# Performance work log

Hardware: AMD Instinct MI355X
Metric: run time of the kernel (lower is better)

Reference implementation:

```python
import jax, jax.numpy as jnp
import numpy as np

STEPS = 100
VTH = 1.0
POOL_TH = 0.75


def _conv(x, w):
    # 5x5 conv, stride 1, pad 2, no bias; NCHW / OIHW
    return jax.lax.conv_general_dilated(
        x, w, window_strides=(1, 1), padding=[(2, 2), (2, 2)],
        dimension_numbers=('NCHW', 'OIHW', 'NCHW'))


def _avgpool2(x):
    s = jax.lax.reduce_window(x, 0.0, jax.lax.add, (1, 1, 2, 2), (1, 1, 2, 2), 'VALID')
    return s * 0.25


def _fire(mem, th):
    # torch.nn.functional.threshold(mem, th, 0): keep values > th, else 0
    ex = jnp.where(mem > th, mem, 0.0)
    mem = mem - ex
    out = (ex > 0).astype(mem.dtype)
    return mem, out


def _ave(output, inp):
    c = inp >= output
    denom = jnp.sum(jnp.where(c, inp, 0.0))
    num = jnp.sum(jnp.where(c, output, 0.0))
    return jnp.where(denom < 1e-3, 1.0, num / denom)


def _ave_p(output, inp):
    denom = jnp.sum(inp)
    return jnp.where(denom < 1e-3, 1.0, jnp.sum(output) / denom)


def setup_inputs() -> dict:
    key = jax.random.key(0)
    k_in, k1, k2, k3, k4 = jax.random.split(key, 5)
    B = 512
    inputdata = jax.random.uniform(k_in, (B, 1, 28, 28), dtype=jnp.float32)
    w1 = jax.random.normal(k1, (20, 1, 5, 5), dtype=jnp.float32) * np.sqrt(2.0 / (5 * 5 * 1))
    w2 = jax.random.normal(k2, (50, 20, 5, 5), dtype=jnp.float32) * np.sqrt(2.0 / (5 * 5 * 20))
    wf0 = jax.random.normal(k3, (200, 2450), dtype=jnp.float32) * np.sqrt(2.0 / 2450)
    wf1 = jax.random.normal(k4, (10, 200), dtype=jnp.float32) * np.sqrt(2.0 / 200)
    return {'inputdata': inputdata, 'w1': w1, 'w2': w2, 'wf0': wf0, 'wf1': wf1}


def _spiking_loop(inputdata, w1, w2, wf0, wf1):
    B = inputdata.shape[0]
    f32 = jnp.float32
    z = lambda *s: jnp.zeros(s, f32)
    carry0 = (
        z(B, 20, 28, 28), z(B, 20, 14, 14), z(B, 50, 14, 14), z(B, 50, 7, 7), z(B, 200),  # membranes
        z(B, 1, 28, 28),                                                                   # Total_input
        z(B, 20, 28, 28), z(B, 20, 28, 28),   # Total_1_output, IF_in_c1
        z(B, 20, 14, 14), z(B, 20, 14, 14),   # Total_p1_output, IF_in_p1
        z(B, 50, 14, 14), z(B, 50, 14, 14),   # Total_2_output, IF_in_c2
        z(B, 50, 7, 7), z(B, 50, 7, 7),       # Total_p2_output, IF_in_p2
        z(B, 200), z(B, 200),                  # Total_f0_output, IF_in_f0
    )

    sgn = jnp.sign(inputdata)
    half = jnp.abs(inputdata) / 2.0

    def step(carry, k):
        (m1, m1s, m2, m2s, mf0, Tin, T1, IFc1, Tp1, IFp1, T2, IFc2, Tp2, IFp2, Tf0, IFf0) = carry
        r = jax.random.uniform(k, inputdata.shape, dtype=f32)
        poisson = (half > r).astype(f32) * sgn
        Tin = Tin + poisson

        a = _conv(poisson, w1)
        m1 = m1 + a
        m1, o = _fire(m1, VTH)            # LIF (l=1 -> membrane unchanged)
        IFc1 = IFc1 + a
        T1 = T1 + o

        a = _avgpool2(o)
        m1s = m1s + a
        m1s, o = _fire(m1s, POOL_TH)
        IFp1 = IFp1 + a
        Tp1 = Tp1 + o

        a = _conv(o, w2)
        m2 = m2 + a
        m2, o = _fire(m2, VTH)
        IFc2 = IFc2 + a
        T2 = T2 + o

        a = _avgpool2(o)
        m2s = m2s + a
        m2s, o = _fire(m2s, POOL_TH)
        IFp2 = IFp2 + a
        Tp2 = Tp2 + o

        a = o.reshape(B, -1) @ wf0.T
        mf0 = mf0 + a
        mf0, o = _fire(mf0, VTH)
        IFf0 = IFf0 + a
        Tf0 = Tf0 + o

        return (m1, m1s, m2, m2s, mf0, Tin, T1, IFc1, Tp1, IFp1, T2, IFc2, Tp2, IFp2, Tf0, IFf0), None

    keys = jax.random.split(jax.random.key(42), STEPS)
    carry, _ = jax.lax.scan(step, carry0, keys)
    return jax.lax.stop_gradient(carry)  # loop ran under torch.no_grad()


def _forward(inputdata, w1, w2, wf0, wf1):
    sg = jax.lax.stop_gradient
    (_, _, _, _, _, Tin, T1, IFc1, Tp1, IFp1, T2, IFc2, Tp2, IFp2, Tf0, IFf0) = \
        _spiking_loop(inputdata, w1, w2, wf0, wf1)

    # global scales start at 1, sign == 1 branch taken
    s1 = 0.6 * _ave(T1, IFc1) + 0.4
    s2 = 0.6 * _ave_p(Tp1, IFp1) + 0.4
    s3 = 0.6 * _ave(T2, IFc2) + 0.4
    s4 = 0.6 * _ave_p(Tp2, IFp2) + 0.4
    s5 = 0.6 * _ave(Tf0, IFf0) + 0.4
    sc1 = s1 * (IFc1 > 0).astype(jnp.float32)
    sc2 = s2 * (IFp1 > 0).astype(jnp.float32)
    sc3 = s3 * (IFc2 > 0).astype(jnp.float32)
    sc4 = s4 * (IFp2 > 0).astype(jnp.float32)
    sc5 = s5 * (IFf0 > 0).astype(jnp.float32)

    # straight-through graph (ASF-BP)
    B = inputdata.shape[0]
    o = _conv(Tin, w1) * sc1
    T1g = o - sg(o) + T1
    o = _avgpool2(T1g) * sc2
    Tp1g = o - sg(o) + Tp1
    o = _conv(Tp1g, w2) * sc3
    T2g = o - sg(o) + T2
    o = _avgpool2(T2g) * sc4
    Tp2g = o - sg(o) + Tp2
    o = (Tp2g.reshape(B, -1) @ wf0.T) * sc5
    Tf0g = o - sg(o) + Tf0
    fc1_in = Tf0g @ wf1.T
    return fc1_in / VTH / STEPS


def reference(inputdata, w1, w2, wf0, wf1):
    return _forward(inputdata, w1, w2, wf0, wf1)
```

## Files before the change

### kernel.cpp

```cpp
#include <hip/hip_runtime.h>
#include <stdint.h>

#define STEPS 100

typedef float f2 __attribute__((ext_vector_type(2)));

__device__ __forceinline__ uint32_t rotl32(uint32_t v, int r) {
  return (v << r) | (v >> (32 - r));
}

__device__ __forceinline__ void tf2x32(uint32_t k0, uint32_t k1,
                                       uint32_t x0, uint32_t x1,
                                       uint32_t& o0, uint32_t& o1) {
  uint32_t ks2 = k0 ^ k1 ^ 0x1BD11BDAu;
  x0 += k0; x1 += k1;
#define RND(r) { x0 += x1; x1 = rotl32(x1, (r)); x1 ^= x0; }
  RND(13) RND(15) RND(26) RND(6)
  x0 += k1;  x1 += ks2 + 1u;
  RND(17) RND(29) RND(16) RND(24)
  x0 += ks2; x1 += k0 + 2u;
  RND(13) RND(15) RND(26) RND(6)
  x0 += k0;  x1 += k1 + 3u;
  RND(17) RND(29) RND(16) RND(24)
  x0 += k1;  x1 += ks2 + 4u;
  RND(13) RND(15) RND(26) RND(6)
  x0 += ks2; x1 += k0 + 5u;
#undef RND
  o0 = x0; o1 = x1;
}

__global__ void keys_k(uint32_t* __restrict__ kb) {
  int i = threadIdx.x;
  if (i < STEPS) {
    uint32_t a, b;
    tf2x32(0u, 42u, 0u, (uint32_t)i, a, b);
    kb[2 * i] = a;
    kb[2 * i + 1] = b;
  }
}

__global__ void wt_k(const float* __restrict__ w2, float* __restrict__ wT2) {
  int i = blockIdx.x * blockDim.x + threadIdx.x;
  if (i >= 50 * 560) return;
  int oc = i / 560, r = i % 560;
  int ic = r / 28, j = r % 28;
  wT2[i] = (j < 25) ? w2[oc * 500 + ic * 25 + j] : 0.f;
}

__global__ void wf0t_k(const float* __restrict__ wf0,
                       float* __restrict__ wf0T) {
  int i = blockIdx.x * blockDim.x + threadIdx.x;
  if (i >= 2450 * 256) return;
  int k = i >> 8, n = i & 255;
  wf0T[i] = (n < 200) ? wf0[n * 2450 + k] : 0.f;
}

template <int KY>
__device__ __forceinline__ void p2s(const float4& q0, const float4& q1,
                                    const float4& q2, const float4& q3,
                                    const float (&wv)[28], f2 (&a)[7]) {
  f2 E[8] = {{q0.x, q0.y}, {q0.z, q0.w}, {q1.x, q1.y}, {q1.z, q1.w},
             {q2.x, q2.y}, {q2.z, q2.w}, {q3.x, q3.y}, {q3.z, q3.w}};
  f2 O[8] = {{q0.y, q0.z}, {q0.w, q1.x}, {q1.y, q1.z}, {q1.w, q2.x},
             {q2.y, q2.z}, {q2.w, q3.x}, {q3.y, q3.z}, {q3.w, 0.f}};
  constexpr int K = KY * 5;
  f2 W;
  W = f2{wv[K + 0], wv[K + 0]};
#pragma unroll
  for (int j = 0; j < 7; ++j) a[j] = __builtin_elementwise_fma(W, E[j], a[j]);
  W = f2{wv[K + 1], wv[K + 1]};
#pragma unroll
  for (int j = 0; j < 7; ++j) a[j] = __builtin_elementwise_fma(W, O[j], a[j]);
  W = f2{wv[K + 2], wv[K + 2]};
#pragma unroll
  for (int j = 0; j < 7; ++j) a[j] = __builtin_elementwise_fma(W, E[j + 1], a[j]);
  W = f2{wv[K + 3], wv[K + 3]};
#pragma unroll
  for (int j = 0; j < 7; ++j) a[j] = __builtin_elementwise_fma(W, O[j + 1], a[j]);
  W = f2{wv[K + 4], wv[K + 4]};
#pragma unroll
  for (int j = 0; j < 6; ++j) a[j] = __builtin_elementwise_fma(W, E[j + 2], a[j]);
}

__global__ __launch_bounds__(512, 2) void step_all_k(
    const float* __restrict__ x, const float* __restrict__ w1,
    const float* __restrict__ wT2, const uint32_t* __restrict__ kb,
    uint32_t* __restrict__ sp2g) {
  __shared__ __align__(16) float  xhs_l[784];
  __shared__ __align__(16) float  pois_l[32 * 34];
  __shared__ __align__(16) float  sp1_l[20 * 18 * 20];
  __shared__ int8_t  s2_l[50 * 196];
  __shared__ __align__(16) float  m2_l[50 * 196];
  __shared__ float    m2s_l[2450];
  __shared__ float    m1s_l[20 * 196];
  __shared__ float    m1stash[512 * 21];

  const int b  = blockIdx.x;
  const int t  = threadIdx.x;
  const int lq = t & 255;
  const int ohu = __builtin_amdgcn_readfirstlane(t >> 8);
  const bool act1 = lq < 196;
  const int qy = lq / 14, qx = lq % 14;
  const bool pair2 = t < 192;
  const bool sing2 = (t >= 192) && (t < 508);
  const int ocP = t / 7;
  const int y0P = 2 * (t % 7);
  const int gS  = 384 + (t - 192);
  const int ocS = gS / 14;
  const int yS  = gS % 14;

  for (int p = t; p < 784; p += 512) {
    xhs_l[p] = x[b * 784 + p] * 0.5f;
  }
  for (int i = t; i < 32 * 34; i += 512) pois_l[i] = 0.f;
  for (int i = t; i < 20 * 360; i += 512) sp1_l[i] = 0.f;
  for (int i = t; i < 50 * 196; i += 512) m2_l[i] = 0.f;
  for (int i = t; i < 2450; i += 512) m2s_l[i] = 0.f;
  for (int i = t; i < 20 * 196; i += 512) m1s_l[i] = 0.f;
  for (int i = t; i < 512 * 21; i += 512) m1stash[i] = 0.f;

  float m1p[2][10];
#pragma unroll
  for (int i = 0; i < 10; ++i) {
    m1p[0][i] = 0.f;
    m1p[1][i] = 0.f;
  }
  __syncthreads();

  {
    uint32_t k0 = kb[0], k1 = kb[1];
    for (int p = t; p < 784; p += 512) {
      uint32_t o0, o1;
      tf2x32(k0, k1, 0u, (uint32_t)(b * 784 + p), o0, o1);
      float r = __uint_as_float(((o0 ^ o1) >> 9) | 0x3F800000u) - 1.0f;
      float v = xhs_l[p];
      pois_l[(p / 28 + 2) * 34 + (p % 28 + 2)] =
          (fabsf(v) > r) ? ((v > 0.f) ? 1.f : -1.f) : 0.f;
    }
  }
  __syncthreads();

#define LDROW(rr, d) {                                                      \
    const float2* _pr = reinterpret_cast<const float2*>(                    \
        &pois_l[(2 * qy + (rr)) * 34 + 2 * qx]);                            \
    float2 _a0 = _pr[0], _a1 = _pr[1], _a2 = _pr[2];                        \
    d[0] = _a0.x; d[1] = _a0.y; d[2] = _a1.x;                               \
    d[3] = _a1.y; d[4] = _a2.x; d[5] = _a2.y; }

#define LD4(icv, rowv, p0, p1, p2, p3) {                                    \
    const float4* _rn = reinterpret_cast<const float4*>(                    \
        sp1_l + (icv) * 360 + (rowv) * 20);                                 \
    p0 = _rn[0]; p1 = _rn[1]; p2 = _rn[2]; p3 = _rn[3]; }

  for (int s = 0; s < STEPS; ++s) {
    if (act1) {
      float rA[6], rB[6];
      LDROW(0, rA)
      LDROW(1, rB)
      float acc[4][10];
#pragma unroll
      for (int tt = 0; tt < 4; ++tt)
#pragma unroll
        for (int i = 0; i < 10; ++i) acc[tt][i] = 0.f;
#pragma unroll
      for (int ky = 0; ky < 5; ++ky) {
#pragma unroll
        for (int kx = 0; kx < 5; ++kx) {
#pragma unroll
          for (int i = 0; i < 10; ++i) {
            float w = w1[(ohu * 10 + i) * 25 + ky * 5 + kx];
            acc[0][i] += w * rA[kx];
            acc[1][i] += w * rA[kx + 1];
            acc[2][i] += w * rB[kx];
            acc[3][i] += w * rB[kx + 1];
          }
        }
        if (ky < 4) {
#pragma unroll
          for (int j = 0; j < 6; ++j) rA[j] = rB[j];
          LDROW(ky + 2, rB)
        }
      }
#pragma unroll
      for (int i = 0; i < 10; ++i) {
        float s4[4];
#pragma unroll
        for (int tt = 0; tt < 2; ++tt) {
          float m = m1p[tt][i] + acc[tt][i];
          float sp = 0.f;
          if (m > 1.0f) { sp = 1.f; m = 0.f; }
          m1p[tt][i] = m;
          s4[tt] = sp;
        }
        {
          float m = m1stash[t * 21 + i] + acc[2][i];
          float sp = 0.f;
          if (m > 1.0f) { sp = 1.f; m = 0.f; }
          m1stash[t * 21 + i] = m;
          s4[2] = sp;
        }
        {
          float m = m1stash[t * 21 + 10 + i] + acc[3][i];
          float sp = 0.f;
          if (m > 1.0f) { sp = 1.f; m = 0.f; }
          m1stash[t * 21 + 10 + i] = m;
          s4[3] = sp;
        }
        float a = 0.25f * (((s4[0] + s4[1]) + s4[2]) + s4[3]);
        int mi = (ohu * 10 + i) * 196 + lq;
        float mm = m1s_l[mi] + a;
        float spp = 0.f;
        if (mm > 0.75f) { spp = 1.f; mm = 0.f; }
        m1s_l[mi] = mm;
        sp1_l[(ohu * 10 + i) * 360 + (qy + 2) * 20 + (qx + 2)] = spp;
      }
    }
    __syncthreads();

    if (pair2) {
      f2 a0[7], a1[7];
#pragma unroll
      for (int j = 0; j < 7; ++j) { a0[j] = f2{0.f, 0.f}; a1[j] = f2{0.f, 0.f}; }
      float4 A0, A1, A2, A3, B0, B1, B2, B3;
      LD4(0, y0P + 0, A0, A1, A2, A3)
      LD4(0, y0P + 1, B0, B1, B2, B3)
#pragma unroll 1
      for (int ic = 0; ic < 20; ++ic) {
        const int icn = (ic < 19) ? ic + 1 : 19;
        float wv[28];
        {
          const float4* wb4 =
              reinterpret_cast<const float4*>(wT2 + ocP * 560 + ic * 28);
#pragma unroll
          for (int j = 0; j < 7; ++j) {
            float4 q = wb4[j];
            wv[4 * j]     = q.x;
            wv[4 * j + 1] = q.y;
            wv[4 * j + 2] = q.z;
            wv[4 * j + 3] = q.w;
          }
        }
        p2s<0>(A0, A1, A2, A3, wv, a0);
        LD4(ic, y0P + 2, A0, A1, A2, A3)
        __builtin_amdgcn_sched_barrier(0);
        p2s<1>(B0, B1, B2, B3, wv, a0);
        p2s<0>(B0, B1, B2, B3, wv, a1);
        LD4(ic, y0P + 3, B0, B1, B2, B3)
        __builtin_amdgcn_sched_barrier(0);
        p2s<2>(A0, A1, A2, A3, wv, a0);
        p2s<1>(A0, A1, A2, A3, wv, a1);
        LD4(ic, y0P + 4, A0, A1, A2, A3)
        __builtin_amdgcn_sched_barrier(0);
        p2s<3>(B0, B1, B2, B3, wv, a0);
        p2s<2>(B0, B1, B2, B3, wv, a1);
        LD4(ic, y0P + 5, B0, B1, B2, B3)
        __builtin_amdgcn_sched_barrier(0);
        p2s<4>(A0, A1, A2, A3, wv, a0);
        p2s<3>(A0, A1, A2, A3, wv, a1);
        LD4(icn, y0P + 0, A0, A1, A2, A3)
        __builtin_amdgcn_sched_barrier(0);
        p2s<4>(B0, B1, B2, B3, wv, a1);
        LD4(icn, y0P + 1, B0, B1, B2, B3)
        __builtin_amdgcn_sched_barrier(0);
      }
#pragma unroll
      for (int j = 0; j < 7; ++j) {
        {
          int li = ocP * 196 + y0P * 14 + 2 * j;
          float m = m2_l[li] + a0[j].x;
          int8_t sp = 0;
          if (m > 1.0f) { sp = 1; m = 0.f; }
          m2_l[li] = m;
          s2_l[li] = sp;
        }
        {
          int li = ocP * 196 + y0P * 14 + 2 * j + 1;
          float m = m2_l[li] + a0[j].y;
          int8_t sp = 0;
          if (m > 1.0f) { sp = 1; m = 0.f; }
          m2_l[li] = m;
          s2_l[li] = sp;
        }
      }
#pragma unroll
      for (int j = 0; j < 7; ++j) {
        {
          int li = ocP * 196 + (y0P + 1) * 14 + 2 * j;
          float m = m2_l[li] + a1[j].x;
          int8_t sp = 0;
          if (m > 1.0f) { sp = 1; m = 0.f; }
          m2_l[li] = m;
          s2_l[li] = sp;
        }
        {
          int li = ocP * 196 + (y0P + 1) * 14 + 2 * j + 1;
          float m = m2_l[li] + a1[j].y;
          int8_t sp = 0;
          if (m > 1.0f) { sp = 1; m = 0.f; }
          m2_l[li] = m;
          s2_l[li] = sp;
        }
      }
    } else if (sing2) {
      f2 a0[7];
#pragma unroll
      for (int j = 0; j < 7; ++j) a0[j] = f2{0.f, 0.f};
      float4 A0, A1, A2, A3, B0, B1, B2, B3;
#pragma unroll 1
      for (int ic = 0; ic < 20; ++ic) {
        float wv[28];
        {
          const float4* wb4 =
              reinterpret_cast<const float4*>(wT2 + ocS * 560 + ic * 28);
#pragma unroll
          for (int j = 0; j < 7; ++j) {
            float4 q = wb4[j];
            wv[4 * j]     = q.x;
            wv[4 * j + 1] = q.y;
            wv[4 * j + 2] = q.z;
            wv[4 * j + 3] = q.w;
          }
        }
        LD4(ic, yS + 0, A0, A1, A2, A3)
        LD4(ic, yS + 1, B0, B1, B2, B3)
        p2s<0>(A0, A1, A2, A3, wv, a0);
        LD4(ic, yS + 2, A0, A1, A2, A3)
        __builtin_amdgcn_sched_barrier(0);
        p2s<1>(B0, B1, B2, B3, wv, a0);
        LD4(ic, yS + 3, B0, B1, B2, B3)
        __builtin_amdgcn_sched_barrier(0);
        p2s<2>(A0, A1, A2, A3, wv, a0);
        LD4(ic, yS + 4, A0, A1, A2, A3)
        __builtin_amdgcn_sched_barrier(0);
        p2s<3>(B0, B1, B2, B3, wv, a0);
        __builtin_amdgcn_sched_barrier(0);
        p2s<4>(A0, A1, A2, A3, wv, a0);
        __builtin_amdgcn_sched_barrier(0);
      }
#pragma unroll
      for (int j = 0; j < 7; ++j) {
        {
          int li = ocS * 196 + yS * 14 + 2 * j;
          float m = m2_l[li] + a0[j].x;
          int8_t sp = 0;
          if (m > 1.0f) { sp = 1; m = 0.f; }
          m2_l[li] = m;
          s2_l[li] = sp;
        }
        {
          int li = ocS * 196 + yS * 14 + 2 * j + 1;
          float m = m2_l[li] + a0[j].y;
          int8_t sp = 0;
          if (m > 1.0f) { sp = 1; m = 0.f; }
          m2_l[li] = m;
          s2_l[li] = sp;
        }
      }
    }
    __syncthreads();

#pragma unroll
    for (int i = 0; i < 5; ++i) {
      int e = i * 512 + t;
      bool fire = false;
      if (e < 2450) {
        int oc = e / 49, qq = e % 49;
        int yo = qq / 7, xo = qq % 7;
        int ib = oc * 196 + 2 * yo * 14 + 2 * xo;
        float s00 = (float)s2_l[ib];
        float s01 = (float)s2_l[ib + 1];
        float s10 = (float)s2_l[ib + 14];
        float s11 = (float)s2_l[ib + 15];
        float a = 0.25f * (((s00 + s01) + s10) + s11);
        float m = m2s_l[e] + a;
        if (m > 0.75f) { fire = true; m = 0.f; }
        m2s_l[e] = m;
      }
      unsigned long long mask = __ballot(fire);
      int base = (e & ~63);
      if ((t & 63) == 0 && base < 2450) {
        int d = base >> 5;
        sp2g[b * 7700 + s * 77 + d] = (uint32_t)mask;
        if (base + 32 < 2450)
          sp2g[b * 7700 + s * 77 + d + 1] = (uint32_t)(mask >> 32);
      }
    }
    if (s + 1 < STEPS) {
      uint32_t k0 = kb[2 * (s + 1)], k1 = kb[2 * (s + 1) + 1];
      for (int p = t; p < 784; p += 512) {
        uint32_t o0, o1;
        tf2x32(k0, k1, 0u, (uint32_t)(b * 784 + p), o0, o1);
        float r = __uint_as_float(((o0 ^ o1) >> 9) | 0x3F800000u) - 1.0f;
        float v = xhs_l[p];
        pois_l[(p / 28 + 2) * 34 + (p % 28 + 2)] =
            (fabsf(v) > r) ? ((v > 0.f) ? 1.f : -1.f) : 0.f;
      }
    }
    __syncthreads();
  }
#undef LDROW
#undef LD4
}

__global__ __launch_bounds__(256) void fc0f_k(
    const uint32_t* __restrict__ sp2g, const float* __restrict__ wf0T,
    float* __restrict__ Tf0g) {
  __shared__ uint32_t mk[77];
  const int b = blockIdx.x;
  const int n = threadIdx.x;
  float m = 0.f, T = 0.f;
  for (int s = 0; s < STEPS; ++s) {
    __syncthreads();
    if (n < 77) mk[n] = sp2g[b * 7700 + s * 77 + n];
    __syncthreads();
    float acc = 0.f;
    for (int d = 0; d < 77; ++d) {
      uint32_t um = mk[d];
      while (um) {
        int j = __builtin_ctz(um);
        um &= um - 1;
        acc += wf0T[((d << 5) + j) * 256 + n];
      }
    }
    m += acc;
    if (m > 1.0f) { T += 1.f; m = 0.f; }
  }
  if (n < 200) Tf0g[b * 200 + n] = T;
}

__global__ void fc1_k(const float* __restrict__ Tf0,
                      const float* __restrict__ wf1,
                      float* __restrict__ out) {
  int idx = blockIdx.x * blockDim.x + threadIdx.x;
  if (idx >= 5120) return;
  int b = idx / 10, i = idx % 10;
  float a = 0.f;
  for (int j = 0; j < 200; ++j) a += Tf0[b * 200 + j] * wf1[i * 200 + j];
  out[idx] = (a / 1.0f) / 100.0f;
}

extern "C" void kernel_launch(void* const* d_in, const int* in_sizes, int n_in,
                              void* d_out, int out_size, void* d_ws, size_t ws_size,
                              hipStream_t stream) {
  (void)in_sizes; (void)n_in; (void)out_size; (void)ws_size;
  const float* x   = (const float*)d_in[0];
  const float* w1  = (const float*)d_in[1];
  const float* w2  = (const float*)d_in[2];
  const float* wf0 = (const float*)d_in[3];
  const float* wf1 = (const float*)d_in[4];
  float* out = (float*)d_out;
  char* ws = (char*)d_ws;

  const size_t tf0_b  = 512ull * 200 * 4;
  const size_t wt_b   = 50ull * 560 * 4;
  const size_t key_b  = 1024;
  const size_t wf0t_b = 2450ull * 256 * 4;
  float*    Tf0g = (float*)ws;
  float*    wT2  = (float*)(ws + tf0_b);
  uint32_t* kb   = (uint32_t*)(ws + tf0_b + wt_b);
  float*    wf0T = (float*)(ws + tf0_b + wt_b + key_b);
  uint32_t* sp2g = (uint32_t*)(ws + tf0_b + wt_b + key_b + wf0t_b);

  keys_k<<<1, 128, 0, stream>>>(kb);
  wt_k<<<110, 256, 0, stream>>>(w2, wT2);
  wf0t_k<<<2450, 256, 0, stream>>>(wf0, wf0T);
  step_all_k<<<512, 512, 0, stream>>>(x, w1, wT2, kb, sp2g);
  fc0f_k<<<512, 256, 0, stream>>>(sp2g, wf0T, Tf0g);
  fc1_k<<<20, 256, 0, stream>>>(Tf0g, wf1, out);
}
```

Baseline: 9.004 ms.

## Fuse 2x2 spike pooling into conv2 epilogue and pack output bits via shared bytes

The conv2 threads now compute pool-2 membrane updates directly from their register-held spikes. Paired-row threads handle both rows themselves, and single-row threads pull the neighbour row's spikes with a shuffle. Each thread writes a 7-bit fire byte to a small shared buffer, and 77 threads then pack these into the 32-bit words stored to global memory. This drops the int8 spike buffer, one block-wide barrier and the separate 2450-element pooling pass per step. The cost is more register pressure and reliance on the neighbour lane holding the odd row.

```diff
diff --git a/kernel.cpp b/kernel.cpp
--- a/kernel.cpp
+++ b/kernel.cpp
@@ -89,11 +89,11 @@
   __shared__ __align__(16) float  xhs_l[784];
   __shared__ __align__(16) float  pois_l[32 * 34];
   __shared__ __align__(16) float  sp1_l[20 * 18 * 20];
-  __shared__ int8_t  s2_l[50 * 196];
   __shared__ __align__(16) float  m2_l[50 * 196];
   __shared__ float    m2s_l[2450];
   __shared__ float    m1s_l[20 * 196];
   __shared__ float    m1stash[512 * 21];
+  __shared__ uint8_t  fb[352];
 
   const int b  = blockIdx.x;
   const int t  = threadIdx.x;
@@ -105,7 +105,7 @@
   const bool sing2 = (t >= 192) && (t < 508);
   const int ocP = t / 7;
   const int y0P = 2 * (t % 7);
-  const int gS  = 384 + (t - 192);
+  const int gS  = 192 + t;
   const int ocS = gS / 14;
   const int yS  = gS % 14;
 
@@ -118,6 +118,7 @@
   for (int i = t; i < 2450; i += 512) m2s_l[i] = 0.f;
   for (int i = t; i < 20 * 196; i += 512) m1s_l[i] = 0.f;
   for (int i = t; i < 512 * 21; i += 512) m1stash[i] = 0.f;
+  if (t < 352) fb[t] = 0;
 
   float m1p[2][10];
 #pragma unroll
@@ -263,23 +264,24 @@
         LD4(icn, y0P + 1, B0, B1, B2, B3)
         __builtin_amdgcn_sched_barrier(0);
       }
+      float f0[14], f1[14];
 #pragma unroll
       for (int j = 0; j < 7; ++j) {
         {
           int li = ocP * 196 + y0P * 14 + 2 * j;
           float m = m2_l[li] + a0[j].x;
-          int8_t sp = 0;
-          if (m > 1.0f) { sp = 1; m = 0.f; }
-          m2_l[li] = m;
-          s2_l[li] = sp;
+          float sp = 0.f;
+          if (m > 1.0f) { sp = 1.f; m = 0.f; }
+          m2_l[li] = m;
+          f0[2 * j] = sp;
         }
         {
           int li = ocP * 196 + y0P * 14 + 2 * j + 1;
           float m = m2_l[li] + a0[j].y;
-          int8_t sp = 0;
-          if (m > 1.0f) { sp = 1; m = 0.f; }
-          m2_l[li] = m;
-          s2_l[li] = sp;
+          float sp = 0.f;
+          if (m > 1.0f) { sp = 1.f; m = 0.f; }
+          m2_l[li] = m;
+          f0[2 * j + 1] = sp;
         }
       }
 #pragma unroll
@@ -287,20 +289,33 @@
         {
           int li = ocP * 196 + (y0P + 1) * 14 + 2 * j;
           float m = m2_l[li] + a1[j].x;
-          int8_t sp = 0;
-          if (m > 1.0f) { sp = 1; m = 0.f; }
-          m2_l[li] = m;
-          s2_l[li] = sp;
+          float sp = 0.f;
+          if (m > 1.0f) { sp = 1.f; m = 0.f; }
+          m2_l[li] = m;
+          f1[2 * j] = sp;
         }
         {
           int li = ocP * 196 + (y0P + 1) * 14 + 2 * j + 1;
           float m = m2_l[li] + a1[j].y;
-          int8_t sp = 0;
-          if (m > 1.0f) { sp = 1; m = 0.f; }
-          m2_l[li] = m;
-          s2_l[li] = sp;
-        }
-      }
+          float sp = 0.f;
+          if (m > 1.0f) { sp = 1.f; m = 0.f; }
+          m2_l[li] = m;
+          f1[2 * j + 1] = sp;
+        }
+      }
+      uint32_t byte = 0;
+#pragma unroll
+      for (int xo = 0; xo < 7; ++xo) {
+        float a = 0.25f * (((f0[2 * xo] + f0[2 * xo + 1]) + f1[2 * xo]) +
+                           f1[2 * xo + 1]);
+        int e = ocP * 49 + (t % 7) * 7 + xo;
+        float m = m2s_l[e] + a;
+        uint32_t bit = 0;
+        if (m > 0.75f) { bit = 1; m = 0.f; }
+        m2s_l[e] = m;
+        byte |= bit << xo;
+      }
+      fb[t] = (uint8_t)byte;
     } else if (sing2) {
       f2 a0[7];
 #pragma unroll
@@ -337,52 +352,47 @@
         p2s<4>(A0, A1, A2, A3, wv, a0);
         __builtin_amdgcn_sched_barrier(0);
       }
+      float sf[14];
+      uint32_t rb = 0;
 #pragma unroll
       for (int j = 0; j < 7; ++j) {
         {
           int li = ocS * 196 + yS * 14 + 2 * j;
           float m = m2_l[li] + a0[j].x;
-          int8_t sp = 0;
-          if (m > 1.0f) { sp = 1; m = 0.f; }
-          m2_l[li] = m;
-          s2_l[li] = sp;
+          float sp = 0.f;
+          if (m > 1.0f) { sp = 1.f; m = 0.f; }
+          m2_l[li] = m;
+          sf[2 * j] = sp;
+          rb |= (sp > 0.f ? 1u : 0u) << (2 * j);
         }
         {
           int li = ocS * 196 + yS * 14 + 2 * j + 1;
           float m = m2_l[li] + a0[j].y;
-          int8_t sp = 0;
-          if (m > 1.0f) { sp = 1; m = 0.f; }
-          m2_l[li] = m;
-          s2_l[li] = sp;
-        }
-      }
-    }
-    __syncthreads();
-
-#pragma unroll
-    for (int i = 0; i < 5; ++i) {
-      int e = i * 512 + t;
-      bool fire = false;
-      if (e < 2450) {
-        int oc = e / 49, qq = e % 49;
-        int yo = qq / 7, xo = qq % 7;
-        int ib = oc * 196 + 2 * yo * 14 + 2 * xo;
-        float s00 = (float)s2_l[ib];
-        float s01 = (float)s2_l[ib + 1];
-        float s10 = (float)s2_l[ib + 14];
-        float s11 = (float)s2_l[ib + 15];
-        float a = 0.25f * (((s00 + s01) + s10) + s11);
-        float m = m2s_l[e] + a;
-        if (m > 0.75f) { fire = true; m = 0.f; }
-        m2s_l[e] = m;
-      }
-      unsigned long long mask = __ballot(fire);
-      int base = (e & ~63);
-      if ((t & 63) == 0 && base < 2450) {
-        int d = base >> 5;
-        sp2g[b * 7700 + s * 77 + d] = (uint32_t)mask;
-        if (base + 32 < 2450)
-          sp2g[b * 7700 + s * 77 + d + 1] = (uint32_t)(mask >> 32);
+          float sp = 0.f;
+          if (m > 1.0f) { sp = 1.f; m = 0.f; }
+          m2_l[li] = m;
+          sf[2 * j + 1] = sp;
+          rb |= (sp > 0.f ? 1u : 0u) << (2 * j + 1);
+        }
+      }
+      uint32_t pb = (uint32_t)__shfl_down((int)rb, 1);
+      if ((yS & 1) == 0) {
+        uint32_t byte = 0;
+#pragma unroll
+        for (int xo = 0; xo < 7; ++xo) {
+          float s00 = sf[2 * xo];
+          float s01 = sf[2 * xo + 1];
+          float s10 = (float)((pb >> (2 * xo)) & 1u);
+          float s11 = (float)((pb >> (2 * xo + 1)) & 1u);
+          float a = 0.25f * (((s00 + s01) + s10) + s11);
+          int e = ocS * 49 + (yS >> 1) * 7 + xo;
+          float m = m2s_l[e] + a;
+          uint32_t bit = 0;
+          if (m > 0.75f) { bit = 1; m = 0.f; }
+          m2s_l[e] = m;
+          byte |= bit << xo;
+        }
+        fb[ocS * 7 + (yS >> 1)] = (uint8_t)byte;
       }
     }
     if (s + 1 < STEPS) {
@@ -397,6 +407,18 @@
       }
     }
     __syncthreads();
+
+    if (t < 77) {
+      int j0 = (32 * t) / 7;
+      uint64_t accw = 0;
+#pragma unroll
+      for (int jj = 0; jj < 6; ++jj) {
+        int j = j0 + jj;
+        uint32_t bv = (j < 350) ? (uint32_t)fb[j] : 0u;
+        accw |= (uint64_t)bv << (7 * j - 32 * t + 6);
+      }
+      sp2g[b * 7700 + s * 77 + t] = (uint32_t)(accw >> 6);
+    }
   }
 #undef LDROW
 #undef LD4
```

New measurement: 8.810 ms, median of 2. 1.02x faster.
